# Performance work log

Hardware: AMD Instinct MI355X
Metric: run time of the kernel (lower is better)

The kernel has to match this reference:

```python
import jax, jax.numpy as jnp
import numpy as np

DIM = 1024
HEADS = 16
DIM_HEAD = 64
SEQ = 2048
BATCH = 2
SCALE = DIM_HEAD ** -0.5
NEG = -jnp.finfo(jnp.float32).max


def setup_inputs() -> dict:
    key = jax.random.key(0)
    k1, k2, k3 = jax.random.split(key, 3)
    x = jax.random.normal(k1, (BATCH, SEQ, DIM), dtype=jnp.float32)
    w_qkv = jax.random.normal(k2, (DIM, 3 * HEADS * DIM_HEAD), dtype=jnp.float32) * 0.02
    w_out = jax.random.normal(k3, (HEADS * DIM_HEAD, DIM), dtype=jnp.float32) * 0.02
    b_out = jnp.zeros((DIM,), dtype=jnp.float32)
    return {"x": x, "w_qkv": w_qkv, "w_out": w_out, "b_out": b_out}


def reference(x, w_qkv, w_out, b_out):
    b, n, _ = x.shape
    qkv = x @ w_qkv  # [b, n, 3*h*d]
    q, k, v = jnp.split(qkv, 3, axis=-1)
    def to_heads(t):
        return t.reshape(b, n, HEADS, DIM_HEAD).transpose(0, 2, 1, 3)  # b h n d
    q, k, v = to_heads(q), to_heads(k), to_heads(v)
    q = q * SCALE
    dots = jnp.einsum('bhid,bhjd->bhij', q, k)  # materialized [b,h,n,n] scores
    causal_mask = jnp.triu(jnp.ones((n, n), dtype=bool), k=1)
    dots = jnp.where(causal_mask, NEG, dots)
    attn = jax.nn.softmax(dots, axis=-1)
    out = jnp.einsum('bhij,bhjd->bhid', attn, v)
    out = out.transpose(0, 2, 1, 3).reshape(b, n, HEADS * DIM_HEAD)
    return out @ w_out + b_out
```

## Files before the change

### kernel.cpp

```cpp
#include <hip/hip_runtime.h>
#include <cstdint>

typedef __attribute__((ext_vector_type(8))) short bfrag_t;
typedef __attribute__((ext_vector_type(4))) float f32x4_t;

#define MFMA16(a,b,c) __builtin_amdgcn_mfma_f32_16x16x32_bf16((a),(b),(c),0,0,0)

__device__ __forceinline__ unsigned short f2bf(float f){
  unsigned u = __float_as_uint(f);
  unsigned r = u + 0x7fffu + ((u >> 16) & 1u);
  return (unsigned short)(r >> 16);
}

__device__ __forceinline__ unsigned pk2bf(float a, float b){
  unsigned r;
  asm("v_cvt_pk_bf16_f32 %0, %1, %2" : "=v"(r) : "v"(a), "v"(b));
  return r;
}

__device__ __forceinline__ void gload16(const unsigned short* g, unsigned short* l){
  __builtin_amdgcn_global_load_lds(
      (const __attribute__((address_space(1))) unsigned int*)(const void*)g,
      (__attribute__((address_space(3))) unsigned int*)(void*)l,
      16, 0, 0);
}

__global__ __launch_bounds__(256) void k_cvt(const float* __restrict__ in,
                                             unsigned short* __restrict__ out, int n4){
  int i = blockIdx.x*blockDim.x + threadIdx.x;
  int stride = gridDim.x*blockDim.x;
  for(; i < n4; i += stride){
    float4 v = ((const float4*)in)[i];
    ushort4 o;
    o.x = f2bf(v.x); o.y = f2bf(v.y); o.z = f2bf(v.z); o.w = f2bf(v.w);
    ((ushort4*)out)[i] = o;
  }
}

__global__ __launch_bounds__(256) void k_transpose(const float* __restrict__ in,
                                                   unsigned short* __restrict__ out,
                                                   int R, int C){
  __shared__ unsigned short tile[32][33];
  int bc = blockIdx.x*32, br = blockIdx.y*32;
  int tx = threadIdx.x & 31, ty = threadIdx.x >> 5;
  #pragma unroll
  for(int i=0;i<32;i+=8){
    tile[ty+i][tx] = f2bf(in[(size_t)(br+ty+i)*C + bc + tx]);
  }
  __syncthreads();
  #pragma unroll
  for(int i=0;i<32;i+=8){
    out[(size_t)(bc+ty+i)*R + br + tx] = tile[tx][ty+i];
  }
}

template<int EPI, int BM>
__global__ __launch_bounds__(256) void k_gemm(
    const unsigned short* __restrict__ A,
    const unsigned short* __restrict__ Bt,
    int M, int N, int K,
    unsigned short* __restrict__ Qo, unsigned short* __restrict__ Kimg,
    unsigned short* __restrict__ Vimg,
    float* __restrict__ Co, const float* __restrict__ bias)
{
  constexpr int WM = (BM==128) ? 2 : 1;
  constexpr int WN = 4/WM;
  constexpr int MI = BM/(16*WM);
  constexpr int NI = 128/(16*WN);

  __shared__ unsigned short ldsA[BM*32];
  __shared__ unsigned short ldsB[128*32];

  const int tid = threadIdx.x;
  const int lane = tid & 63;
  const int w = tid >> 6;
  const int wr = w / WN, wc = w % WN;
  const int col16 = lane & 15, g = lane >> 4;

  const int bm = blockIdx.y * BM;
  const int bn = blockIdx.x * 128;

  f32x4_t acc[MI][NI];
  #pragma unroll
  for(int i=0;i<MI;i++)
    #pragma unroll
    for(int j=0;j<NI;j++) acc[i][j] = (f32x4_t)0.0f;

  for(int k0=0; k0<K; k0+=32){
    __syncthreads();
    #pragma unroll
    for(int i=0; i<BM*4/256; i++){
      int u = i*256 + tid;
      int row = u>>2, s = u&3, gs = s ^ ((row>>1)&3);
      gload16(A + (size_t)(bm+row)*K + k0 + gs*8, ldsA + (i*256 + w*64)*8);
    }
    #pragma unroll
    for(int i=0; i<2; i++){
      int u = i*256 + tid;
      int row = u>>2, s = u&3, gs = s ^ ((row>>1)&3);
      gload16(Bt + (size_t)(bn+row)*K + k0 + gs*8, ldsB + (i*256 + w*64)*8);
    }
    __syncthreads();
    bfrag_t af[MI], bfr[NI];
    #pragma unroll
    for(int mi=0;mi<MI;mi++){
      int row = wr*(MI*16) + mi*16 + col16;
      int slot = g ^ ((row>>1)&3);
      af[mi] = *(const bfrag_t*)(ldsA + row*32 + slot*8);
    }
    #pragma unroll
    for(int ni=0;ni<NI;ni++){
      int row = wc*(NI*16) + ni*16 + col16;
      int slot = g ^ ((row>>1)&3);
      bfr[ni] = *(const bfrag_t*)(ldsB + row*32 + slot*8);
    }
    #pragma unroll
    for(int mi=0;mi<MI;mi++)
      #pragma unroll
      for(int ni=0;ni<NI;ni++)
        acc[mi][ni] = MFMA16(af[mi], bfr[ni], acc[mi][ni]);
  }

  if (EPI == 0){
    #pragma unroll
    for(int mi=0;mi<MI;mi++){
      int mrow = bm + wr*(MI*16) + mi*16 + g*4;
      #pragma unroll
      for(int ni=0;ni<NI;ni++){
        int ncol = bn + wc*(NI*16) + ni*16 + col16;
        int which = ncol >> 10, rem = ncol & 1023;
        int h = rem >> 6, d = rem & 63;
        #pragma unroll
        for(int r=0;r<4;r++){
          int m_ = mrow + r;
          int b = m_ >> 11, sq = m_ & 2047;
          size_t bh = (size_t)(b*16 + h);
          float v = acc[mi][ni][r];
          if (which == 0){
            Qo[(bh*2048 + sq)*64 + d] = f2bf(v * 0.125f);
          } else if (which == 1){
            int kt = sq >> 6, rr = sq & 63;
            int ks = rr >> 4, c16 = rr & 15;
            int dk = d >> 5, g3 = (d >> 3) & 3, e = d & 7;
            size_t off = bh*131072 + (size_t)kt*4096
                       + (size_t)(ks*2 + dk)*512 + (size_t)(g3*16 + c16)*8 + e;
            Kimg[off] = f2bf(v);
          } else {
            int kt = sq >> 6, sc = sq & 63;
            int jk = sc >> 5, g3 = (sc >> 3) & 3, e = sc & 7;
            int n = d >> 4, c16 = d & 15;
            size_t off = bh*131072 + (size_t)kt*4096
                       + (size_t)(n*2 + jk)*512 + (size_t)(g3*16 + c16)*8 + e;
            Vimg[off] = f2bf(v);
          }
        }
      }
    }
  } else {
    #pragma unroll
    for(int mi=0;mi<MI;mi++){
      int mrow = bm + wr*(MI*16) + mi*16 + g*4;
      #pragma unroll
      for(int ni=0;ni<NI;ni++){
        int ncol = bn + wc*(NI*16) + ni*16 + col16;
        float bb = bias[ncol];
        #pragma unroll
        for(int r=0;r<4;r++){
          Co[(size_t)(mrow+r)*N + ncol] = acc[mi][ni][r] + bb;
        }
      }
    }
  }
}

__global__ __launch_bounds__(256, 4) void k_attn(
    const unsigned short* __restrict__ Q,
    const unsigned short* __restrict__ Kimg,
    const unsigned short* __restrict__ Vimg,
    unsigned short* __restrict__ O)
{
  __shared__ unsigned short kls[2*4096];
  __shared__ unsigned short vls[2*4096];
  __shared__ unsigned short plds[4*1024];
  const int lane = threadIdx.x & 63;
  const int w = threadIdx.x >> 6;
  const int col16 = lane & 15, g = lane >> 4;
  const int bh = blockIdx.x;
  const int qt = 31 - blockIdx.y;
  const int b = bh >> 4, h = bh & 15;

  const unsigned short* Qb = Q    + (size_t)bh*2048*64;
  const unsigned short* Kb = Kimg + (size_t)bh*131072;
  const unsigned short* Vb = Vimg + (size_t)bh*131072;
  char* pw = (char*)(plds + w*1024);

  auto stage = [&](int kt, int bsel){
    const unsigned short* gk = Kb + (size_t)kt*4096;
    const unsigned short* gv = Vb + (size_t)kt*4096;
    unsigned short* lk = kls + bsel*4096;
    unsigned short* lv = vls + bsel*4096;
    #pragma unroll
    for(int c=0;c<2;c++){
      int chunk = w*2 + c;
      int u = chunk*64 + lane;
      gload16(gk + u*8, lk + chunk*512);
      gload16(gv + u*8, lv + chunk*512);
    }
  };

  const int qrow0 = qt*64 + w*16;
  const int nkt = qt + 1;
  const int qi = qrow0 + col16;

  bfrag_t qf[2];
  #pragma unroll
  for(int dk=0;dk<2;dk++)
    qf[dk] = *(const bfrag_t*)(Qb + (size_t)(qrow0 + col16)*64 + dk*32 + g*8);

  f32x4_t oaccT[4];
  #pragma unroll
  for(int n=0;n<4;n++) oaccT[n] = (f32x4_t)0.0f;
  float mrun = -1e30f, lrun = 0.f;

  stage(0, 0);
  __syncthreads();

  #pragma unroll 1
  for(int kt=0; kt<nkt; kt++){
    const int cur = kt & 1;
    if (kt+1 < nkt) stage(kt+1, cur^1);

    const bfrag_t* kb = (const bfrag_t*)(kls + cur*4096);
    const bfrag_t* vb = (const bfrag_t*)(vls + cur*4096);

    f32x4_t sacc[4];
    #pragma unroll
    for(int ks=0; ks<4; ks++){
      bfrag_t kf0 = kb[(ks*2+0)*64 + lane];
      bfrag_t kf1 = kb[(ks*2+1)*64 + lane];
      f32x4_t c = (f32x4_t)0.0f;
      c = MFMA16(kf0, qf[0], c);
      c = MFMA16(kf1, qf[1], c);
      sacc[ks] = c;
    }
    if (kt == qt){
      const int kbase = kt*64;
      #pragma unroll
      for(int ks=0; ks<4; ks++)
        #pragma unroll
        for(int r=0;r<4;r++){
          int kj = kbase + ks*16 + g*4 + r;
          if (kj > qi) sacc[ks][r] = -1e30f;
        }
    }
    float pm = fmaxf(
        fmaxf(fmaxf(fmaxf(sacc[0][0],sacc[0][1]),fmaxf(sacc[0][2],sacc[0][3])),
              fmaxf(fmaxf(sacc[1][0],sacc[1][1]),fmaxf(sacc[1][2],sacc[1][3]))),
        fmaxf(fmaxf(fmaxf(sacc[2][0],sacc[2][1]),fmaxf(sacc[2][2],sacc[2][3])),
              fmaxf(fmaxf(sacc[3][0],sacc[3][1]),fmaxf(sacc[3][2],sacc[3][3]))));
    pm = fmaxf(pm, __shfl_xor(pm, 16));
    pm = fmaxf(pm, __shfl_xor(pm, 32));
    if (!__all(pm - mrun <= 8.0f)){
      float mnew = fmaxf(mrun, pm);
      float alpha = __expf(mrun - mnew);
      mrun = mnew;
      lrun *= alpha;
      #pragma unroll
      for(int n=0;n<4;n++)
        #pragma unroll
        for(int r=0;r<4;r++)
          oaccT[n][r] *= alpha;
    }
    float rs = 0.f;
    #pragma unroll
    for(int ks=0; ks<4; ks++){
      float p0 = __expf(sacc[ks][0] - mrun);
      float p1 = __expf(sacc[ks][1] - mrun);
      float p2 = __expf(sacc[ks][2] - mrun);
      float p3 = __expf(sacc[ks][3] - mrun);
      rs += (p0+p1)+(p2+p3);
      unsigned w0 = pk2bf(p0, p1);
      unsigned w1 = pk2bf(p2, p3);
      int byte0 = (col16*128 + (ks*16 + g*4)*2) ^ ((col16&7)<<4);
      *(unsigned*)(pw + byte0)     = w0;
      *(unsigned*)(pw + byte0 + 4) = w1;
    }
    rs += __shfl_xor(rs, 16);
    rs += __shfl_xor(rs, 32);
    lrun += rs;
    bfrag_t pf[2];
    #pragma unroll
    for(int jk=0;jk<2;jk++){
      int byteo = (col16*128 + jk*64 + g*16) ^ ((col16&7)<<4);
      pf[jk] = *(const bfrag_t*)(pw + byteo);
    }
    #pragma unroll
    for(int n=0;n<4;n++){
      bfrag_t v0 = vb[(n*2+0)*64 + lane];
      bfrag_t v1 = vb[(n*2+1)*64 + lane];
      oaccT[n] = MFMA16(v0, pf[0], oaccT[n]);
      oaccT[n] = MFMA16(v1, pf[1], oaccT[n]);
    }
    __syncthreads();
  }

  {
    float inv = 1.0f / lrun;
    size_t obase = ((size_t)(b*2048 + qi))*1024 + (size_t)h*64;
    #pragma unroll
    for(int n=0;n<4;n++){
      unsigned w0 = pk2bf(oaccT[n][0]*inv, oaccT[n][1]*inv);
      unsigned w1 = pk2bf(oaccT[n][2]*inv, oaccT[n][3]*inv);
      uint2 pkd; pkd.x = w0; pkd.y = w1;
      *(uint2*)(O + obase + n*16 + g*4) = pkd;
    }
  }
}

extern "C" void kernel_launch(void* const* d_in, const int* in_sizes, int n_in,
                              void* d_out, int out_size, void* d_ws, size_t ws_size,
                              hipStream_t stream){
  const float* x     = (const float*)d_in[0];
  const float* w_qkv = (const float*)d_in[1];
  const float* w_out = (const float*)d_in[2];
  const float* b_out = (const float*)d_in[3];
  float* out = (float*)d_out;

  unsigned char* ws = (unsigned char*)d_ws;
  unsigned short* xbf   = (unsigned short*)(ws);
  unsigned short* wqkvT = (unsigned short*)(ws + (size_t)8*1024*1024);
  unsigned short* woutT = (unsigned short*)(ws + (size_t)14*1024*1024);
  unsigned short* Qb    = (unsigned short*)(ws + (size_t)16*1024*1024);
  unsigned short* Kb    = (unsigned short*)(ws + (size_t)24*1024*1024);
  unsigned short* Vtb   = (unsigned short*)(ws + (size_t)32*1024*1024);
  unsigned short* attno = xbf;

  k_cvt<<<2048, 256, 0, stream>>>(x, xbf, 4096*1024/4);
  k_transpose<<<dim3(3072/32, 1024/32), 256, 0, stream>>>(w_qkv, wqkvT, 1024, 3072);
  k_transpose<<<dim3(1024/32, 1024/32), 256, 0, stream>>>(w_out, woutT, 1024, 1024);
  k_gemm<0,128><<<dim3(24, 32), 256, 0, stream>>>(xbf, wqkvT, 4096, 3072, 1024,
                                                  Qb, Kb, Vtb, nullptr, nullptr);
  k_attn<<<dim3(32, 32), 256, 0, stream>>>(Qb, Kb, Vtb, attno);
  k_gemm<1,64><<<dim3(8, 64), 256, 0, stream>>>(attno, woutT, 4096, 1024, 1024,
                                                nullptr, nullptr, nullptr, out, b_out);
}
```

Baseline: 122.7 us.

## Vectorize GEMM epilogues via swapped MFMA operands, split QKV GEMM, use exp2 softmax

New measurement: 152.8 us. 1.25x slower.

```diff
diff --git a/kernel.cpp b/kernel.cpp
--- a/kernel.cpp
+++ b/kernel.cpp
@@ -54,11 +54,11 @@
   }
 }
 
-template<int EPI, int BM>
+template<int EPI, int BM, int SWAP>
 __global__ __launch_bounds__(256) void k_gemm(
     const unsigned short* __restrict__ A,
     const unsigned short* __restrict__ Bt,
-    int M, int N, int K,
+    int M, int N, int K, int bnoff,
     unsigned short* __restrict__ Qo, unsigned short* __restrict__ Kimg,
     unsigned short* __restrict__ Vimg,
     float* __restrict__ Co, const float* __restrict__ bias)
@@ -78,7 +78,7 @@
   const int col16 = lane & 15, g = lane >> 4;
 
   const int bm = blockIdx.y * BM;
-  const int bn = blockIdx.x * 128;
+  const int bn = blockIdx.x * 128 + bnoff;
 
   f32x4_t acc[MI][NI];
   #pragma unroll
@@ -117,57 +117,79 @@
     #pragma unroll
     for(int mi=0;mi<MI;mi++)
       #pragma unroll
-      for(int ni=0;ni<NI;ni++)
-        acc[mi][ni] = MFMA16(af[mi], bfr[ni], acc[mi][ni]);
+      for(int ni=0;ni<NI;ni++){
+        if (SWAP) acc[mi][ni] = MFMA16(bfr[ni], af[mi], acc[mi][ni]);
+        else      acc[mi][ni] = MFMA16(af[mi], bfr[ni], acc[mi][ni]);
+      }
   }
 
   if (EPI == 0){
-    #pragma unroll
-    for(int mi=0;mi<MI;mi++){
-      int mrow = bm + wr*(MI*16) + mi*16 + g*4;
-      #pragma unroll
-      for(int ni=0;ni<NI;ni++){
-        int ncol = bn + wc*(NI*16) + ni*16 + col16;
-        int which = ncol >> 10, rem = ncol & 1023;
-        int h = rem >> 6, d = rem & 63;
+    if (SWAP){
+      const int which = bn >> 10;
+      #pragma unroll
+      for(int mi=0;mi<MI;mi++){
+        int s_full = bm + wr*(MI*16) + mi*16 + col16;
+        int b = s_full >> 11, sq = s_full & 2047;
         #pragma unroll
-        for(int r=0;r<4;r++){
-          int m_ = mrow + r;
-          int b = m_ >> 11, sq = m_ & 2047;
+        for(int ni=0;ni<NI;ni++){
+          int n0 = bn + wc*(NI*16) + ni*16 + g*4;
+          int h = (n0 & 1023) >> 6;
+          int d0 = n0 & 63;
           size_t bh = (size_t)(b*16 + h);
-          float v = acc[mi][ni][r];
+          float v0 = acc[mi][ni][0], v1 = acc[mi][ni][1];
+          float v2 = acc[mi][ni][2], v3 = acc[mi][ni][3];
           if (which == 0){
-            Qo[(bh*2048 + sq)*64 + d] = f2bf(v * 0.125f);
-          } else if (which == 1){
+            const float sc = 0.18033688f;
+            uint2 pkd; pkd.x = pk2bf(v0*sc, v1*sc); pkd.y = pk2bf(v2*sc, v3*sc);
+            *(uint2*)(Qo + (bh*2048 + sq)*64 + d0) = pkd;
+          } else {
             int kt = sq >> 6, rr = sq & 63;
-            int ks = rr >> 4, c16 = rr & 15;
-            int dk = d >> 5, g3 = (d >> 3) & 3, e = d & 7;
+            int ks = rr >> 4, c16i = rr & 15;
+            int dk = d0 >> 5, g3 = (d0 >> 3) & 3, e0 = d0 & 7;
+            uint2 pkd; pkd.x = pk2bf(v0, v1); pkd.y = pk2bf(v2, v3);
             size_t off = bh*131072 + (size_t)kt*4096
-                       + (size_t)(ks*2 + dk)*512 + (size_t)(g3*16 + c16)*8 + e;
-            Kimg[off] = f2bf(v);
-          } else {
-            int kt = sq >> 6, sc = sq & 63;
-            int jk = sc >> 5, g3 = (sc >> 3) & 3, e = sc & 7;
-            int n = d >> 4, c16 = d & 15;
-            size_t off = bh*131072 + (size_t)kt*4096
-                       + (size_t)(n*2 + jk)*512 + (size_t)(g3*16 + c16)*8 + e;
-            Vimg[off] = f2bf(v);
+                       + (size_t)(ks*2 + dk)*512 + (size_t)(g3*16 + c16i)*8 + e0;
+            *(uint2*)(Kimg + off) = pkd;
           }
         }
       }
+    } else {
+      #pragma unroll
+      for(int mi=0;mi<MI;mi++){
+        int s0 = bm + wr*(MI*16) + mi*16 + g*4;
+        int b = s0 >> 11, sq0 = s0 & 2047;
+        int kt = sq0 >> 6, sc0 = sq0 & 63;
+        int jk = sc0 >> 5, g3 = (sc0 >> 3) & 3, e0 = sc0 & 7;
+        #pragma unroll
+        for(int ni=0;ni<NI;ni++){
+          int ncol = bn + wc*(NI*16) + ni*16 + col16;
+          int h = (ncol & 1023) >> 6;
+          int d64 = ncol & 63;
+          int nimg = d64 >> 4, c16i = d64 & 15;
+          size_t bh = (size_t)(b*16 + h);
+          uint2 pkd;
+          pkd.x = pk2bf(acc[mi][ni][0], acc[mi][ni][1]);
+          pkd.y = pk2bf(acc[mi][ni][2], acc[mi][ni][3]);
+          size_t off = bh*131072 + (size_t)kt*4096
+                     + (size_t)(nimg*2 + jk)*512 + (size_t)(g3*16 + c16i)*8 + e0;
+          *(uint2*)(Vimg + off) = pkd;
+        }
+      }
     }
   } else {
     #pragma unroll
     for(int mi=0;mi<MI;mi++){
-      int mrow = bm + wr*(MI*16) + mi*16 + g*4;
+      int m = bm + wr*(MI*16) + mi*16 + col16;
       #pragma unroll
       for(int ni=0;ni<NI;ni++){
-        int ncol = bn + wc*(NI*16) + ni*16 + col16;
-        float bb = bias[ncol];
-        #pragma unroll
-        for(int r=0;r<4;r++){
-          Co[(size_t)(mrow+r)*N + ncol] = acc[mi][ni][r] + bb;
-        }
+        int n0 = bn + wc*(NI*16) + ni*16 + g*4;
+        float4 bb = *(const float4*)(bias + n0);
+        float4 o;
+        o.x = acc[mi][ni][0] + bb.x;
+        o.y = acc[mi][ni][1] + bb.y;
+        o.z = acc[mi][ni][2] + bb.z;
+        o.w = acc[mi][ni][3] + bb.w;
+        *(float4*)(Co + (size_t)m*N + n0) = o;
       }
     }
   }
@@ -186,7 +208,8 @@
   const int w = threadIdx.x >> 6;
   const int col16 = lane & 15, g = lane >> 4;
   const int bh = blockIdx.x;
-  const int qt = 31 - blockIdx.y;
+  const int y = blockIdx.y;
+  const int qt = (y & 1) ? (y >> 1) : (31 - (y >> 1));
   const int b = bh >> 4, h = bh & 15;
 
   const unsigned short* Qb = Q    + (size_t)bh*2048*64;
@@ -260,9 +283,9 @@
               fmaxf(fmaxf(sacc[3][0],sacc[3][1]),fmaxf(sacc[3][2],sacc[3][3]))));
     pm = fmaxf(pm, __shfl_xor(pm, 16));
     pm = fmaxf(pm, __shfl_xor(pm, 32));
-    if (!__all(pm - mrun <= 8.0f)){
+    if (!__all(pm - mrun <= 11.5415603f)){
       float mnew = fmaxf(mrun, pm);
-      float alpha = __expf(mrun - mnew);
+      float alpha = __builtin_amdgcn_exp2f(mrun - mnew);
       mrun = mnew;
       lrun *= alpha;
       #pragma unroll
@@ -274,16 +297,16 @@
     float rs = 0.f;
     #pragma unroll
     for(int ks=0; ks<4; ks++){
-      float p0 = __expf(sacc[ks][0] - mrun);
-      float p1 = __expf(sacc[ks][1] - mrun);
-      float p2 = __expf(sacc[ks][2] - mrun);
-      float p3 = __expf(sacc[ks][3] - mrun);
+      float p0 = __builtin_amdgcn_exp2f(sacc[ks][0] - mrun);
+      float p1 = __builtin_amdgcn_exp2f(sacc[ks][1] - mrun);
+      float p2 = __builtin_amdgcn_exp2f(sacc[ks][2] - mrun);
+      float p3 = __builtin_amdgcn_exp2f(sacc[ks][3] - mrun);
       rs += (p0+p1)+(p2+p3);
       unsigned w0 = pk2bf(p0, p1);
       unsigned w1 = pk2bf(p2, p3);
       int byte0 = (col16*128 + (ks*16 + g*4)*2) ^ ((col16&7)<<4);
-      *(unsigned*)(pw + byte0)     = w0;
-      *(unsigned*)(pw + byte0 + 4) = w1;
+      unsigned long long wd = ((unsigned long long)w1 << 32) | w0;
+      *(unsigned long long*)(pw + byte0) = wd;
     }
     rs += __shfl_xor(rs, 16);
     rs += __shfl_xor(rs, 32);
@@ -309,9 +332,9 @@
     size_t obase = ((size_t)(b*2048 + qi))*1024 + (size_t)h*64;
     #pragma unroll
     for(int n=0;n<4;n++){
-      unsigned w0 = pk2bf(oaccT[n][0]*inv, oaccT[n][1]*inv);
-      unsigned w1 = pk2bf(oaccT[n][2]*inv, oaccT[n][3]*inv);
-      uint2 pkd; pkd.x = w0; pkd.y = w1;
+      uint2 pkd;
+      pkd.x = pk2bf(oaccT[n][0]*inv, oaccT[n][1]*inv);
+      pkd.y = pk2bf(oaccT[n][2]*inv, oaccT[n][3]*inv);
       *(uint2*)(O + obase + n*16 + g*4) = pkd;
     }
   }
@@ -338,9 +361,11 @@
   k_cvt<<<2048, 256, 0, stream>>>(x, xbf, 4096*1024/4);
   k_transpose<<<dim3(3072/32, 1024/32), 256, 0, stream>>>(w_qkv, wqkvT, 1024, 3072);
   k_transpose<<<dim3(1024/32, 1024/32), 256, 0, stream>>>(w_out, woutT, 1024, 1024);
-  k_gemm<0,128><<<dim3(24, 32), 256, 0, stream>>>(xbf, wqkvT, 4096, 3072, 1024,
-                                                  Qb, Kb, Vtb, nullptr, nullptr);
+  k_gemm<0,128,1><<<dim3(16, 32), 256, 0, stream>>>(xbf, wqkvT, 4096, 3072, 1024, 0,
+                                                    Qb, Kb, Vtb, nullptr, nullptr);
+  k_gemm<0,128,0><<<dim3(8, 32), 256, 0, stream>>>(xbf, wqkvT, 4096, 3072, 1024, 2048,
+                                                   Qb, Kb, Vtb, nullptr, nullptr);
   k_attn<<<dim3(32, 32), 256, 0, stream>>>(Qb, Kb, Vtb, attno);
-  k_gemm<1,64><<<dim3(8, 64), 256, 0, stream>>>(attno, woutT, 4096, 1024, 1024,
-                                                nullptr, nullptr, nullptr, out, b_out);
-}
+  k_gemm<1,64,1><<<dim3(8, 64), 256, 0, stream>>>(attno, woutT, 4096, 1024, 1024, 0,
+                                                  nullptr, nullptr, nullptr, out, b_out);
+}
```
